# Optimization experiments

Measured on AMD Instinct MI355X. Metric: run time of the kernel, lower is better.

## Reference

```python
import jax, jax.numpy as jnp
import numpy as np

NUM_SEQS = 8
SEQ_LEN = 2048
HIDDEN = 768
NUM_HEADS = 12
HEAD_DIM = 64
EPS = 1e-12


def setup_inputs() -> dict:
    key = jax.random.key(0)
    ks = jax.random.split(key, 12)
    total = NUM_SEQS * SEQ_LEN
    hidden_states = jax.random.normal(ks[0], (total, HIDDEN), dtype=jnp.float32)
    cu_seq_lens = jnp.arange(NUM_SEQS + 1, dtype=jnp.int32) * SEQ_LEN
    s = 0.02
    inp = {
        "hidden_states": hidden_states,
        "cu_seq_lens": cu_seq_lens,
        "max_seq_len": SEQ_LEN,
        "norm_w": jnp.ones((HIDDEN,), jnp.float32),
        "norm_b": jnp.zeros((HIDDEN,), jnp.float32),
        "Wq": jax.random.normal(ks[1], (HIDDEN, HIDDEN), jnp.float32) * s,
        "bq": jnp.zeros((HIDDEN,), jnp.float32),
        "Wk": jax.random.normal(ks[2], (HIDDEN, HIDDEN), jnp.float32) * s,
        "bk": jnp.zeros((HIDDEN,), jnp.float32),
        "Wv": jax.random.normal(ks[3], (HIDDEN, HIDDEN), jnp.float32) * s,
        "bv": jnp.zeros((HIDDEN,), jnp.float32),
        "Wo": jax.random.normal(ks[4], (HIDDEN, HIDDEN), jnp.float32) * s,
        "bo": jnp.zeros((HIDDEN,), jnp.float32),
    }
    return inp


def _layer_norm(x, w, b):
    mu = jnp.mean(x, axis=-1, keepdims=True)
    var = jnp.mean(jnp.square(x - mu), axis=-1, keepdims=True)
    return (x - mu) * jax.lax.rsqrt(var + EPS) * w + b


def _rope(x, positions, interleaved=False):
    # x: [t, h, d]; positions: [t]
    d = x.shape[-1]
    inv_freq = 1.0 / (10000.0 ** (jnp.arange(0, d, 2, dtype=jnp.float32) / d))  # [d/2]
    theta = positions.astype(jnp.float32)[:, None] * inv_freq[None, :]  # [t, d/2]
    cos = jnp.cos(theta)[:, None, :]  # [t, 1, d/2]
    sin = jnp.sin(theta)[:, None, :]
    x1, x2 = x[..., : d // 2], x[..., d // 2 :]
    return jnp.concatenate([x1 * cos - x2 * sin, x2 * cos + x1 * sin], axis=-1)


def _attention(q, k, v):
    # q,k,v: [b, s, h, d] (equal-length sequences, no padding)
    scale = 1.0 / jnp.sqrt(jnp.asarray(q.shape[-1], q.dtype))
    scores = jnp.einsum("bqhd,bkhd->bhqk", q, k) * scale
    probs = jax.nn.softmax(scores, axis=-1)
    return jnp.einsum("bhqk,bkhd->bqhd", probs, v)


def reference(hidden_states, cu_seq_lens, max_seq_len, norm_w, norm_b,
              Wq, bq, Wk, bk, Wv, bv, Wo, bo):
    t = hidden_states.shape[0]
    # pre_norm, layer_idx=1 -> LayerNorm
    x = _layer_norm(hidden_states, norm_w, norm_b)
    value = x @ Wv + bv
    query = x @ Wq + bq
    key = x @ Wk + bk

    def split(z):
        return z.reshape(t, NUM_HEADS, HEAD_DIM)

    q, k, v = split(query), split(key), split(value)

    # positions within each sequence (equal-length packing)
    positions = jnp.tile(jnp.arange(SEQ_LEN, dtype=jnp.int32), NUM_SEQS)
    q = _rope(q, positions)
    k = _rope(k, positions)

    # reshape packed -> [b, s, h, d]; sequences are equal-length here
    qb = q.reshape(NUM_SEQS, SEQ_LEN, NUM_HEADS, HEAD_DIM)
    kb = k.reshape(NUM_SEQS, SEQ_LEN, NUM_HEADS, HEAD_DIM)
    vb = v.reshape(NUM_SEQS, SEQ_LEN, NUM_HEADS, HEAD_DIM)
    attn = _attention(qb, kb, vb).reshape(t, HIDDEN)

    attn = attn @ Wo + bo
    # residual add (dropout prob = 0)
    out = attn + x
    return out
```

## Files before the change

### kernel.cpp

```cpp
#include <hip/hip_runtime.h>

typedef __bf16 bf16x8 __attribute__((ext_vector_type(8)));
typedef float  f32x4  __attribute__((ext_vector_type(4)));

#define MFMA16(a,b,c) __builtin_amdgcn_mfma_f32_16x16x32_bf16((a),(b),(c),0,0,0)

constexpr int  HID  = 768;
constexpr long T    = 16384;
constexpr long SZ   = T * HID;
constexpr int  SEQ  = 2048;
constexpr int  NH   = 12;
constexpr int  HD   = 64;
constexpr int  WELE = HID * HID;

constexpr float QSCALE = 0.125f * 1.4426950408889634f;
constexpr float L10K32 = 13.287712379549449f / 32.0f;

__device__ __forceinline__ unsigned pkbf(float a, float b) {
    union { __bf16 h[2]; unsigned u; } x;
    x.h[0] = (__bf16)a; x.h[1] = (__bf16)b; return x.u;
}

__device__ __forceinline__ void gld16(const __bf16* g, __bf16* l) {
    __builtin_amdgcn_global_load_lds(
        (const __attribute__((address_space(1))) unsigned int*)g,
        (__attribute__((address_space(3))) unsigned int*)l, 16, 0, 0);
}

__global__ __launch_bounds__(256)
void wconv_kernel(const float* __restrict__ W0, __bf16* __restrict__ T0,
                  const float* __restrict__ W1, __bf16* __restrict__ T1,
                  const float* __restrict__ W2, __bf16* __restrict__ T2,
                  const float* __restrict__ W3, __bf16* __restrict__ T3) {
    const float* W; __bf16* Wt;
    switch (blockIdx.z) {
        case 0: W = W0; Wt = T0; break;
        case 1: W = W1; Wt = T1; break;
        case 2: W = W2; Wt = T2; break;
        default: W = W3; Wt = T3; break;
    }
    __shared__ float tile[64][65];
    int n0 = blockIdx.x * 64, k0 = blockIdx.y * 64;
    int c = threadIdx.x & 63, rr = threadIdx.x >> 6;
#pragma unroll
    for (int i = 0; i < 16; i++) {
        int r = i * 4 + rr;
        tile[r][c] = W[(long)(k0 + r) * HID + n0 + c];
    }
    __syncthreads();
#pragma unroll
    for (int i = 0; i < 16; i++) {
        int r = i * 4 + rr;
        Wt[(long)(n0 + r) * HID + k0 + c] = (__bf16)tile[c][r];
    }
}

__global__ __launch_bounds__(256)
void ln_kernel(const float* __restrict__ hs, const float* __restrict__ w,
               const float* __restrict__ b, __bf16* __restrict__ xbf) {
    int row = blockIdx.x, tid = threadIdx.x;
    const float* hr = hs + (long)row * HID;
    float v0 = hr[tid], v1 = hr[tid + 256], v2 = hr[tid + 512];
    float s  = v0 + v1 + v2;
    float s2 = v0 * v0 + v1 * v1 + v2 * v2;
#pragma unroll
    for (int off = 1; off < 64; off <<= 1) {
        s  += __shfl_xor(s, off);
        s2 += __shfl_xor(s2, off);
    }
    __shared__ float red[8];
    int wave = tid >> 6;
    if ((tid & 63) == 0) { red[wave] = s; red[4 + wave] = s2; }
    __syncthreads();
    s  = red[0] + red[1] + red[2] + red[3];
    s2 = red[4] + red[5] + red[6] + red[7];
    float mu   = s * (1.0f / HID);
    float var  = s2 * (1.0f / HID) - mu * mu;
    float rstd = rsqrtf(var + 1e-12f);
    long base = (long)row * HID;
    xbf[base + tid]       = (__bf16)((v0 - mu) * rstd * w[tid]       + b[tid]);
    xbf[base + tid + 256] = (__bf16)((v1 - mu) * rstd * w[tid + 256] + b[tid + 256]);
    xbf[base + tid + 512] = (__bf16)((v2 - mu) * rstd * w[tid + 512] + b[tid + 512]);
}

constexpr int SEGSZ = 528;

template <int MODE>
__global__ __launch_bounds__(256)
void gemm_lds(const __bf16* __restrict__ A, const __bf16* __restrict__ Bt,
              const float* __restrict__ bias, __bf16* __restrict__ outb,
              const __bf16* __restrict__ resid, float* __restrict__ outf,
              float scale) {
    int tid = threadIdx.x, wave = tid >> 6, lane = tid & 63;
    int lr = lane & 15, quad = lane >> 4;
    int wm = wave >> 1, wn = wave & 1;
    long m0 = (long)blockIdx.x * 128;
    int  n0 = blockIdx.y * 128;

    __shared__ __align__(16) __bf16 As[16 * SEGSZ];
    __shared__ __align__(16) __bf16 Bs[16 * SEGSZ];

    const f32x4 vzero = {0.f, 0.f, 0.f, 0.f};
    f32x4 acc[4][4];
#pragma unroll
    for (int ms = 0; ms < 4; ms++)
#pragma unroll
        for (int ns = 0; ns < 4; ns++) acc[ms][ns] = vzero;

    const __bf16* ga = A  + (long)(m0 + wave * 32 + (lane >> 3)) * HID + (lane & 7) * 8;
    const __bf16* gb = Bt + (long)(n0 + wave * 32 + (lane >> 3)) * HID + (lane & 7) * 8;
    __bf16* la = As + wave * 4 * SEGSZ;
    __bf16* lb = Bs + wave * 4 * SEGSZ;

    int fbase = (lr >> 3) * SEGSZ + (lr & 7) * 64 + quad * 8;

    for (int k0 = 0; k0 < HID; k0 += 64) {
#pragma unroll
        for (int j = 0; j < 4; j++) {
            gld16(ga + (long)j * 8 * HID + k0, la + j * SEGSZ);
            gld16(gb + (long)j * 8 * HID + k0, lb + j * SEGSZ);
        }
        __syncthreads();
#pragma unroll
        for (int kk = 0; kk < 64; kk += 32) {
            bf16x8 af[4], bfr[4];
#pragma unroll
            for (int ms = 0; ms < 4; ms++)
                af[ms] = *(const bf16x8*)&As[fbase + (wm * 8 + ms * 2) * SEGSZ + kk];
#pragma unroll
            for (int ns = 0; ns < 4; ns++)
                bfr[ns] = *(const bf16x8*)&Bs[fbase + (wn * 8 + ns * 2) * SEGSZ + kk];
#pragma unroll
            for (int ms = 0; ms < 4; ms++)
#pragma unroll
                for (int ns = 0; ns < 4; ns++)
                    acc[ms][ns] = MFMA16(af[ms], bfr[ns], acc[ms][ns]);
        }
        __syncthreads();
    }

    if (MODE == 3) {
        int hb = n0 + wn * 64;
        float f1 = __builtin_amdgcn_exp2f(-(float)lr * L10K32);
        float f2 = __builtin_amdgcn_exp2f(-(float)(lr + 16) * L10K32);
        float b0 = bias[hb + lr],      b1 = bias[hb + 16 + lr];
        float b2 = bias[hb + 32 + lr], b3 = bias[hb + 48 + lr];
#pragma unroll
        for (int ms = 0; ms < 4; ms++)
#pragma unroll
        for (int r = 0; r < 4; r++) {
            long row = m0 + wm * 64 + ms * 16 + quad * 4 + r;
            int pos = (int)(row & (SEQ - 1));
            float s1, c1, s2, c2;
            __sincosf((float)pos * f1, &s1, &c1);
            __sincosf((float)pos * f2, &s2, &c2);
            float v0 = acc[ms][0][r] + b0, v1 = acc[ms][1][r] + b1;
            float v2 = acc[ms][2][r] + b2, v3 = acc[ms][3][r] + b3;
            __bf16* ob = outb + row * HID + hb;
            ob[lr]      = (__bf16)((v0 * c1 - v2 * s1) * scale);
            ob[16 + lr] = (__bf16)((v1 * c2 - v3 * s2) * scale);
            ob[32 + lr] = (__bf16)((v2 * c1 + v0 * s1) * scale);
            ob[48 + lr] = (__bf16)((v3 * c2 + v1 * s2) * scale);
        }
    } else if (MODE == 1) {
#pragma unroll
        for (int ms = 0; ms < 4; ms++)
#pragma unroll
        for (int r = 0; r < 4; r++) {
            int d = (int)(m0 + wm * 64 + ms * 16 + quad * 4 + r);
            float bv = bias[d];
            int hh = d >> 6, dd = d & 63;
#pragma unroll
            for (int ns = 0; ns < 4; ns++) {
                int posg = n0 + wn * 64 + ns * 16 + lr;
                int sq = posg >> 11, pos = posg & (SEQ - 1);
                outb[((long)((sq * NH + hh) * HD + dd) << 11) + pos] =
                    (__bf16)(acc[ms][ns][r] + bv);
            }
        }
    } else {
#pragma unroll
        for (int ns = 0; ns < 4; ns++) {
            int col = n0 + wn * 64 + ns * 16 + lr;
            float bv = bias[col];
#pragma unroll
            for (int ms = 0; ms < 4; ms++)
#pragma unroll
            for (int r = 0; r < 4; r++) {
                long row = m0 + wm * 64 + ms * 16 + quad * 4 + r;
                outf[row * HID + col] = acc[ms][ns][r] + bv + (float)resid[row * HID + col];
            }
        }
    }
}

__global__ __launch_bounds__(256)
void attn_kernel(const __bf16* __restrict__ q, const __bf16* __restrict__ k,
                 const __bf16* __restrict__ vt, __bf16* __restrict__ att) {
    int tid = threadIdx.x, wave = tid >> 6, lane = tid & 63;
    int lr = lane & 15, quad = lane >> 4;
    int bb = blockIdx.x;
    int s  = bb & 7;
    int ii = bb >> 3;
    int h  = ii >> 4;
    int qt = ii & 15;
    long q0 = (long)s * SEQ + qt * 128 + wave * 32;

    __shared__ __align__(16) __bf16 Ks[2][128 * 64];
    __shared__ __align__(16) __bf16 Vs[2][64 * 128];
    __shared__ __align__(16) __bf16 Ps[4][32][40];

    const f32x4 vzero = {0.f, 0.f, 0.f, 0.f};

    bf16x8 qf[2][2];
#pragma unroll
    for (int m = 0; m < 2; m++) {
        const __bf16* qrow = q + (q0 + m * 16 + lr) * HID + h * HD + quad * 8;
        qf[m][0] = *(const bf16x8*)(qrow);
        qf[m][1] = *(const bf16x8*)(qrow + 32);
    }

    f32x4 o[2][4];
#pragma unroll
    for (int m = 0; m < 2; m++)
#pragma unroll
        for (int d = 0; d < 4; d++) o[m][d] = vzero;
    float m_i[2]  = {-INFINITY, -INFINITY};
    float lsum[2] = {0.f, 0.f};

    const __bf16* kg = k  + (long)s * SEQ * HID + h * HD;
    const __bf16* vg = vt + (long)(s * NH + h) * HD * SEQ;

#define STAGE(bufi, kpos)                                                          \
    {                                                                              \
        _Pragma("unroll")                                                          \
        for (int j = 0; j < 4; j++) {                                              \
            int kr_ = wave * 32 + j * 8 + (lane >> 3);                             \
            gld16(kg + (long)((kpos) + kr_) * HID + (((lane & 7) ^ (kr_ & 7)) << 3), \
                  &Ks[bufi][(wave * 32 + j * 8) * 64]);                            \
            int vr_ = wave * 16 + j * 4 + (lane >> 4);                             \
            gld16(vg + (long)vr_ * SEQ + (kpos) + (((lane & 15) ^ (vr_ & 7)) << 3),  \
                  &Vs[bufi][(wave * 16 + j * 4) * 128]);                           \
        }                                                                          \
    }

    STAGE(0, 0)
    __syncthreads();

    for (int kt = 0; kt < SEQ / 128; kt++) {
        int cur = kt & 1;
        if (kt < SEQ / 128 - 1) STAGE(cur ^ 1, (kt + 1) * 128)

        f32x4 st[2][8];
#pragma unroll
        for (int jt = 0; jt < 8; jt++) {
            const __bf16* krow = &Ks[cur][(jt * 16 + lr) * 64];
            bf16x8 kf0 = *(const bf16x8*)&krow[((quad)     ^ (lr & 7)) << 3];
            bf16x8 kf1 = *(const bf16x8*)&krow[((4 + quad) ^ (lr & 7)) << 3];
#pragma unroll
            for (int m = 0; m < 2; m++) {
                f32x4 t0 = MFMA16(kf0, qf[m][0], vzero);
                st[m][jt] = MFMA16(kf1, qf[m][1], t0);
            }
        }

        float alpha[2];
#pragma unroll
        for (int m = 0; m < 2; m++) {
            f32x4 mx4 = st[m][0];
#pragma unroll
            for (int jt = 1; jt < 8; jt++) {
                mx4[0] = fmaxf(mx4[0], st[m][jt][0]);
                mx4[1] = fmaxf(mx4[1], st[m][jt][1]);
                mx4[2] = fmaxf(mx4[2], st[m][jt][2]);
                mx4[3] = fmaxf(mx4[3], st[m][jt][3]);
            }
            float mx = fmaxf(fmaxf(mx4[0], mx4[1]), fmaxf(mx4[2], mx4[3]));
            mx = fmaxf(mx, __shfl_xor(mx, 16));
            mx = fmaxf(mx, __shfl_xor(mx, 32));
            float nm = fmaxf(m_i[m], mx);
            alpha[m] = __builtin_amdgcn_exp2f(m_i[m] - nm);
            m_i[m] = nm;
            lsum[m] *= alpha[m];
#pragma unroll
            for (int d = 0; d < 4; d++) o[m][d] *= alpha[m];
        }

#pragma unroll
        for (int g = 0; g < 4; g++) {
#pragma unroll
            for (int m = 0; m < 2; m++) {
                float rs = 0.f;
#pragma unroll
                for (int jj = 0; jj < 2; jj++) {
                    int jt = g * 2 + jj;
                    float e0 = __builtin_amdgcn_exp2f(st[m][jt][0] - m_i[m]);
                    float e1 = __builtin_amdgcn_exp2f(st[m][jt][1] - m_i[m]);
                    float e2 = __builtin_amdgcn_exp2f(st[m][jt][2] - m_i[m]);
                    float e3 = __builtin_amdgcn_exp2f(st[m][jt][3] - m_i[m]);
                    rs += (e0 + e1) + (e2 + e3);
                    unsigned long long pw =
                        ((unsigned long long)pkbf(e2, e3) << 32) | pkbf(e0, e1);
                    *(unsigned long long*)&Ps[wave][m * 16 + lr][jj * 16 + quad * 4] = pw;
                }
                lsum[m] += rs;
            }
            asm volatile("s_waitcnt lgkmcnt(0)" ::: "memory");
            bf16x8 vf[4];
#pragma unroll
            for (int d = 0; d < 4; d++)
                vf[d] = *(const bf16x8*)
                    &Vs[cur][(d * 16 + lr) * 128 + (((g * 4 + quad) ^ (lr & 7)) << 3)];
#pragma unroll
            for (int m = 0; m < 2; m++) {
                bf16x8 pb = *(const bf16x8*)&Ps[wave][m * 16 + lr][quad * 8];
#pragma unroll
                for (int d = 0; d < 4; d++) o[m][d] = MFMA16(vf[d], pb, o[m][d]);
            }
        }
        __syncthreads();
    }
#undef STAGE

#pragma unroll
    for (int m = 0; m < 2; m++) {
        float l = lsum[m];
        l += __shfl_xor(l, 16);
        l += __shfl_xor(l, 32);
        float inv = 1.0f / l;
        long row = q0 + m * 16 + lr;
        __bf16* ob = att + row * HID + h * HD + quad * 4;
#pragma unroll
        for (int d = 0; d < 4; d++) {
            unsigned p0 = pkbf(o[m][d][0] * inv, o[m][d][1] * inv);
            unsigned p1 = pkbf(o[m][d][2] * inv, o[m][d][3] * inv);
            *(unsigned*)&ob[d * 16]     = p0;
            *(unsigned*)&ob[d * 16 + 2] = p1;
        }
    }
}

extern "C" void kernel_launch(void* const* d_in, const int* in_sizes, int n_in,
                              void* d_out, int out_size, void* d_ws, size_t ws_size,
                              hipStream_t stream) {
    const float* hs    = (const float*)d_in[0];
    const float* normw = (const float*)d_in[3];
    const float* normb = (const float*)d_in[4];
    const float* Wq = (const float*)d_in[5];
    const float* bq = (const float*)d_in[6];
    const float* Wk = (const float*)d_in[7];
    const float* bk = (const float*)d_in[8];
    const float* Wv = (const float*)d_in[9];
    const float* bv = (const float*)d_in[10];
    const float* Wo = (const float*)d_in[11];
    const float* bo = (const float*)d_in[12];

    __bf16* base = (__bf16*)d_ws;
    __bf16* x   = base;
    __bf16* qb  = base + SZ;
    __bf16* kb  = base + 2 * SZ;
    __bf16* vtb = base + 3 * SZ;
    __bf16* att = base + 4 * SZ;
    __bf16* wqt = base + 5 * SZ;
    __bf16* wkt = wqt + WELE;
    __bf16* wvt = wkt + WELE;
    __bf16* wot = wvt + WELE;

    wconv_kernel<<<dim3(12, 12, 4), 256, 0, stream>>>(Wq, wqt, Wk, wkt, Wv, wvt, Wo, wot);

    ln_kernel<<<(int)T, 256, 0, stream>>>(hs, normw, normb, x);

    gemm_lds<3><<<dim3(T / 128, HID / 128), 256, 0, stream>>>(x, wqt, bq, qb, nullptr, nullptr, QSCALE);
    gemm_lds<3><<<dim3(T / 128, HID / 128), 256, 0, stream>>>(x, wkt, bk, kb, nullptr, nullptr, 1.0f);
    gemm_lds<1><<<dim3(HID / 128, T / 128), 256, 0, stream>>>(wvt, x, bv, vtb, nullptr, nullptr, 1.0f);

    attn_kernel<<<dim3(NH * 16 * 8), 256, 0, stream>>>(qb, kb, vtb, att);

    gemm_lds<2><<<dim3(T / 128, HID / 128), 256, 0, stream>>>(att, wot, bo, nullptr, x, (float*)d_out, 1.0f);
}
```

Measured before the change: 451.2 us.

## Rewrite attention with 32x32 MFMA, register P via shuffles, lazy rescale

Rebuilds the attention inner loop around 32x32x16 bf16 MFMAs with 64-key tiles instead of 128-key tiles. The probability matrix now stays in registers and is rearranged with cross-half lane shuffles, replacing the per-wave LDS scratch round-trip and its waitcnt. It also skips the online-softmax rescale unless the running max grows by more than a threshold, and raises wave priority around the MFMA blocks. Smaller tiles double the number of loop iterations and barriers. The deferred rescale lets exponents exceed 1 by up to 2^8, which could reduce bf16 precision of P.

```diff
diff --git a/kernel.cpp b/kernel.cpp
--- a/kernel.cpp
+++ b/kernel.cpp
@@ -2,8 +2,10 @@
 
 typedef __bf16 bf16x8 __attribute__((ext_vector_type(8)));
 typedef float  f32x4  __attribute__((ext_vector_type(4)));
+typedef float  f32x16 __attribute__((ext_vector_type(16)));
 
 #define MFMA16(a,b,c) __builtin_amdgcn_mfma_f32_16x16x32_bf16((a),(b),(c),0,0,0)
+#define MFMA32(a,b,c) __builtin_amdgcn_mfma_f32_32x32x16_bf16((a),(b),(c),0,0,0)
 
 constexpr int  HID  = 768;
 constexpr long T    = 16384;
@@ -198,7 +200,7 @@
 void attn_kernel(const __bf16* __restrict__ q, const __bf16* __restrict__ k,
                  const __bf16* __restrict__ vt, __bf16* __restrict__ att) {
     int tid = threadIdx.x, wave = tid >> 6, lane = tid & 63;
-    int lr = lane & 15, quad = lane >> 4;
+    int c = lane & 31, hi = lane >> 5;
     int bb = blockIdx.x;
     int s  = bb & 7;
     int ii = bb >> 3;
@@ -206,138 +208,143 @@
     int qt = ii & 15;
     long q0 = (long)s * SEQ + qt * 128 + wave * 32;
 
-    __shared__ __align__(16) __bf16 Ks[2][128 * 64];
-    __shared__ __align__(16) __bf16 Vs[2][64 * 128];
-    __shared__ __align__(16) __bf16 Ps[4][32][40];
-
-    const f32x4 vzero = {0.f, 0.f, 0.f, 0.f};
-
-    bf16x8 qf[2][2];
-#pragma unroll
-    for (int m = 0; m < 2; m++) {
-        const __bf16* qrow = q + (q0 + m * 16 + lr) * HID + h * HD + quad * 8;
-        qf[m][0] = *(const bf16x8*)(qrow);
-        qf[m][1] = *(const bf16x8*)(qrow + 32);
-    }
-
-    f32x4 o[2][4];
-#pragma unroll
-    for (int m = 0; m < 2; m++)
-#pragma unroll
-        for (int d = 0; d < 4; d++) o[m][d] = vzero;
-    float m_i[2]  = {-INFINITY, -INFINITY};
-    float lsum[2] = {0.f, 0.f};
+    __shared__ __align__(16) __bf16 Ks[2][64 * 64];
+    __shared__ __align__(16) __bf16 Vs[2][64 * 64];
+
+    bf16x8 qf[4];
+    {
+        const __bf16* qrow = q + (q0 + c) * HID + h * HD + hi * 8;
+#pragma unroll
+        for (int kk = 0; kk < 4; kk++)
+            qf[kk] = *(const bf16x8*)(qrow + kk * 16);
+    }
+
+    f32x16 o[2] = {};
+    float m_i = -INFINITY, ls = 0.f;
 
     const __bf16* kg = k  + (long)s * SEQ * HID + h * HD;
     const __bf16* vg = vt + (long)(s * NH + h) * HD * SEQ;
 
-#define STAGE(bufi, kpos)                                                          \
-    {                                                                              \
-        _Pragma("unroll")                                                          \
-        for (int j = 0; j < 4; j++) {                                              \
-            int kr_ = wave * 32 + j * 8 + (lane >> 3);                             \
-            gld16(kg + (long)((kpos) + kr_) * HID + (((lane & 7) ^ (kr_ & 7)) << 3), \
-                  &Ks[bufi][(wave * 32 + j * 8) * 64]);                            \
-            int vr_ = wave * 16 + j * 4 + (lane >> 4);                             \
-            gld16(vg + (long)vr_ * SEQ + (kpos) + (((lane & 15) ^ (vr_ & 7)) << 3),  \
-                  &Vs[bufi][(wave * 16 + j * 4) * 128]);                           \
-        }                                                                          \
+    int srow = lane >> 3;
+    int sgch = (lane & 7) ^ srow;
+
+#define STAGE(bufi, kv)                                                         \
+    {                                                                           \
+        _Pragma("unroll")                                                       \
+        for (int rr = 0; rr < 2; rr++) {                                        \
+            int grp = rr * 4 + wave;                                            \
+            gld16(kg + (long)((kv) + grp * 8 + srow) * HID + sgch * 8,          \
+                  &Ks[bufi][grp * 8 * 64]);                                     \
+            gld16(vg + (long)(grp * 8 + srow) * SEQ + (kv) + sgch * 8,          \
+                  &Vs[bufi][grp * 8 * 64]);                                     \
+        }                                                                       \
     }
 
     STAGE(0, 0)
     __syncthreads();
 
-    for (int kt = 0; kt < SEQ / 128; kt++) {
+    for (int kt = 0; kt < SEQ / 64; kt++) {
         int cur = kt & 1;
-        if (kt < SEQ / 128 - 1) STAGE(cur ^ 1, (kt + 1) * 128)
-
-        f32x4 st[2][8];
-#pragma unroll
-        for (int jt = 0; jt < 8; jt++) {
-            const __bf16* krow = &Ks[cur][(jt * 16 + lr) * 64];
-            bf16x8 kf0 = *(const bf16x8*)&krow[((quad)     ^ (lr & 7)) << 3];
-            bf16x8 kf1 = *(const bf16x8*)&krow[((4 + quad) ^ (lr & 7)) << 3];
-#pragma unroll
-            for (int m = 0; m < 2; m++) {
-                f32x4 t0 = MFMA16(kf0, qf[m][0], vzero);
-                st[m][jt] = MFMA16(kf1, qf[m][1], t0);
-            }
-        }
-
-        float alpha[2];
-#pragma unroll
-        for (int m = 0; m < 2; m++) {
-            f32x4 mx4 = st[m][0];
-#pragma unroll
-            for (int jt = 1; jt < 8; jt++) {
-                mx4[0] = fmaxf(mx4[0], st[m][jt][0]);
-                mx4[1] = fmaxf(mx4[1], st[m][jt][1]);
-                mx4[2] = fmaxf(mx4[2], st[m][jt][2]);
-                mx4[3] = fmaxf(mx4[3], st[m][jt][3]);
-            }
-            float mx = fmaxf(fmaxf(mx4[0], mx4[1]), fmaxf(mx4[2], mx4[3]));
-            mx = fmaxf(mx, __shfl_xor(mx, 16));
-            mx = fmaxf(mx, __shfl_xor(mx, 32));
-            float nm = fmaxf(m_i[m], mx);
-            alpha[m] = __builtin_amdgcn_exp2f(m_i[m] - nm);
-            m_i[m] = nm;
-            lsum[m] *= alpha[m];
-#pragma unroll
-            for (int d = 0; d < 4; d++) o[m][d] *= alpha[m];
-        }
-
-#pragma unroll
-        for (int g = 0; g < 4; g++) {
-#pragma unroll
-            for (int m = 0; m < 2; m++) {
-                float rs = 0.f;
-#pragma unroll
-                for (int jj = 0; jj < 2; jj++) {
-                    int jt = g * 2 + jj;
-                    float e0 = __builtin_amdgcn_exp2f(st[m][jt][0] - m_i[m]);
-                    float e1 = __builtin_amdgcn_exp2f(st[m][jt][1] - m_i[m]);
-                    float e2 = __builtin_amdgcn_exp2f(st[m][jt][2] - m_i[m]);
-                    float e3 = __builtin_amdgcn_exp2f(st[m][jt][3] - m_i[m]);
-                    rs += (e0 + e1) + (e2 + e3);
-                    unsigned long long pw =
-                        ((unsigned long long)pkbf(e2, e3) << 32) | pkbf(e0, e1);
-                    *(unsigned long long*)&Ps[wave][m * 16 + lr][jj * 16 + quad * 4] = pw;
+        if (kt < SEQ / 64 - 1) STAGE(cur ^ 1, (kt + 1) * 64)
+
+        f32x16 st[2];
+        __builtin_amdgcn_s_setprio(1);
+#pragma unroll
+        for (int kh = 0; kh < 2; kh++) {
+            f32x16 acc = {};
+            int R = kh * 32 + c;
+#pragma unroll
+            for (int kk = 0; kk < 4; kk++) {
+                bf16x8 kf = *(const bf16x8*)
+                    &Ks[cur][R * 64 + ((((kk << 1) + hi) ^ (R & 7)) << 3)];
+                acc = MFMA32(kf, qf[kk], acc);
+            }
+            st[kh] = acc;
+        }
+        __builtin_amdgcn_s_setprio(0);
+
+        float pmax = st[0][0];
+#pragma unroll
+        for (int r = 1; r < 16; r++) pmax = fmaxf(pmax, st[0][r]);
+#pragma unroll
+        for (int r = 0; r < 16; r++) pmax = fmaxf(pmax, st[1][r]);
+        pmax = fmaxf(pmax, __shfl_xor(pmax, 32));
+        if (__any(pmax > m_i + 8.0f)) {
+            float nm = fmaxf(m_i, pmax);
+            float alpha = __builtin_amdgcn_exp2f(m_i - nm);
+            m_i = nm;
+            ls *= alpha;
+#pragma unroll
+            for (int dh = 0; dh < 2; dh++)
+#pragma unroll
+                for (int r = 0; r < 16; r++) o[dh][r] *= alpha;
+        }
+        float rs = 0.f;
+#pragma unroll
+        for (int kh = 0; kh < 2; kh++)
+#pragma unroll
+            for (int r = 0; r < 16; r++) {
+                float e = __builtin_amdgcn_exp2f(st[kh][r] - m_i);
+                st[kh][r] = e;
+                rs += e;
+            }
+        ls += rs;
+
+        bf16x8 pb[4];
+#pragma unroll
+        for (int kh = 0; kh < 2; kh++) {
+            unsigned pk[8];
+#pragma unroll
+            for (int i = 0; i < 8; i++)
+                pk[i] = pkbf(st[kh][2 * i], st[kh][2 * i + 1]);
+#pragma unroll
+            for (int b = 0; b < 2; b++) {
+                unsigned w[4];
+#pragma unroll
+                for (int wl = 0; wl < 2; wl++) {
+                    unsigned p0 = pk[4 * b + wl];
+                    unsigned p1 = pk[4 * b + 2 + wl];
+                    unsigned sel = hi ? p0 : p1;
+                    unsigned t = (unsigned)__shfl_xor((int)sel, 32);
+                    w[wl]     = hi ? t : p0;
+                    w[2 + wl] = hi ? p1 : t;
                 }
-                lsum[m] += rs;
-            }
-            asm volatile("s_waitcnt lgkmcnt(0)" ::: "memory");
-            bf16x8 vf[4];
-#pragma unroll
-            for (int d = 0; d < 4; d++)
-                vf[d] = *(const bf16x8*)
-                    &Vs[cur][(d * 16 + lr) * 128 + (((g * 4 + quad) ^ (lr & 7)) << 3)];
-#pragma unroll
-            for (int m = 0; m < 2; m++) {
-                bf16x8 pb = *(const bf16x8*)&Ps[wave][m * 16 + lr][quad * 8];
-#pragma unroll
-                for (int d = 0; d < 4; d++) o[m][d] = MFMA16(vf[d], pb, o[m][d]);
-            }
-        }
+                union { unsigned u[4]; bf16x8 v; } pu;
+                pu.u[0] = w[0]; pu.u[1] = w[1]; pu.u[2] = w[2]; pu.u[3] = w[3];
+                pb[2 * kh + b] = pu.v;
+            }
+        }
+
+        __builtin_amdgcn_s_setprio(1);
+#pragma unroll
+        for (int dh = 0; dh < 2; dh++) {
+            int R = dh * 32 + c;
+#pragma unroll
+            for (int kk = 0; kk < 4; kk++) {
+                bf16x8 vf = *(const bf16x8*)
+                    &Vs[cur][R * 64 + ((((kk << 1) + hi) ^ (R & 7)) << 3)];
+                o[dh] = MFMA32(vf, pb[kk], o[dh]);
+            }
+        }
+        __builtin_amdgcn_s_setprio(0);
+
         __syncthreads();
     }
 #undef STAGE
 
-#pragma unroll
-    for (int m = 0; m < 2; m++) {
-        float l = lsum[m];
-        l += __shfl_xor(l, 16);
-        l += __shfl_xor(l, 32);
-        float inv = 1.0f / l;
-        long row = q0 + m * 16 + lr;
-        __bf16* ob = att + row * HID + h * HD + quad * 4;
-#pragma unroll
-        for (int d = 0; d < 4; d++) {
-            unsigned p0 = pkbf(o[m][d][0] * inv, o[m][d][1] * inv);
-            unsigned p1 = pkbf(o[m][d][2] * inv, o[m][d][3] * inv);
-            *(unsigned*)&ob[d * 16]     = p0;
-            *(unsigned*)&ob[d * 16 + 2] = p1;
-        }
-    }
+    ls += __shfl_xor(ls, 32);
+    float inv = 1.0f / ls;
+    __bf16* ob = att + (q0 + c) * HID + h * HD;
+#pragma unroll
+    for (int dh = 0; dh < 2; dh++)
+#pragma unroll
+        for (int a = 0; a < 4; a++) {
+            unsigned lo  = pkbf(o[dh][4 * a] * inv,     o[dh][4 * a + 1] * inv);
+            unsigned hi2 = pkbf(o[dh][4 * a + 2] * inv, o[dh][4 * a + 3] * inv);
+            int d = dh * 32 + a * 8 + hi * 4;
+            *(unsigned long long*)&ob[d] =
+                ((unsigned long long)hi2 << 32) | lo;
+        }
 }
 
 extern "C" void kernel_launch(void* const* d_in, const int* in_sizes, int n_in,
```

New measurement: 451.9 us. No clear change (+0.1%).
